# Kernel optimization log

Hardware: AMD Instinct MI355X
Metric: run time of the kernel (lower is better)

The kernel has to match this reference:

```python
import jax, jax.numpy as jnp
import numpy as np

NEG_INF = -9e16
SLOPE = 0.2  # leaky relu slope


def setup_inputs() -> dict:
    key = jax.random.key(0)
    k1, k2, k3, k4 = jax.random.split(key, 4)
    N, F_in, H, D = 3072, 512, 8, 64
    h = jax.random.normal(k1, (N, F_in), dtype=jnp.float32)
    adj = jax.random.randint(k2, (N, N), 0, 2, dtype=jnp.int32)
    W = jax.random.normal(k3, (H, F_in, D), dtype=jnp.float32) * (2.0 / (F_in + D)) ** 0.5
    a = jax.random.normal(k4, (H, 2 * D, 1), dtype=jnp.float32) * (2.0 / (2 * D + 1)) ** 0.5
    return {"h": h, "adj": adj, "W": W, "a": a}


def reference(h, adj, W, a):
    # h: [N, F], W: [H, F, D], a: [H, 2D, 1], adj: [N, N]
    H, _, D = W.shape
    ht = jnp.einsum("nf,hfd->hnd", h, W)            # [H, N, D]
    a_src = a[:, :D, 0]                               # [H, D]
    a_dst = a[:, D:, 0]                               # [H, D]
    src = jnp.einsum("hnd,hd->hn", ht, a_src)        # [H, N]
    dst = jnp.einsum("hnd,hd->hn", ht, a_dst)        # [H, N]
    e = src[:, :, None] + dst[:, None, :]             # [H, N, N]
    e = jnp.where(e > 0, e, SLOPE * e)                # leaky relu
    e = jnp.where(adj[None] > 0, e, NEG_INF)
    att = jax.nn.softmax(e, axis=-1)                  # [H, N, N]
    hp = jnp.einsum("hnm,hmd->hnd", att, ht)         # [H, N, D]
    out = jnp.transpose(hp, (1, 0, 2)).reshape(h.shape[0], H * D)  # concat heads
    return (out, att)
```

## Files before the change

kernel.cpp:

```cpp
#include <hip/hip_runtime.h>

#define NN 3072
#define FF 512
#define HH 8
#define DD 64
#define SLOPEV 0.2f
#define CH2 64
#define NC2 (NN/CH2)

typedef __bf16  bf16x8 __attribute__((ext_vector_type(8)));
typedef __bf16  bf16x4 __attribute__((ext_vector_type(4)));
typedef short   s16x8  __attribute__((ext_vector_type(8)));
typedef float   f32x4  __attribute__((ext_vector_type(4)));
typedef unsigned long long u64;

#define MFMA16(a,b,c) __builtin_amdgcn_mfma_f32_16x16x32_bf16((a),(b),(c),0,0,0)

__device__ __forceinline__ short f2bf(float x){ __bf16 b=(__bf16)x; return __builtin_bit_cast(short,b); }
__device__ __forceinline__ float bf2f(short s){ return (float)__builtin_bit_cast(__bf16,s); }
__device__ __forceinline__ bf16x8 ldbf8(const short* p){ return __builtin_bit_cast(bf16x8, *(const s16x8*)p); }

__device__ __forceinline__ void gload16(const void* g, void* l){
  __builtin_amdgcn_global_load_lds(
      (const __attribute__((address_space(1))) void*)(uintptr_t)g,
      (__attribute__((address_space(3))) void*)(uint32_t)(uintptr_t)l, 16, 0, 0);
}

__global__ __launch_bounds__(64) void k_wt(const float* __restrict__ W, const float* __restrict__ a,
    short* __restrict__ wthi, short* __restrict__ wtlo,
    float* __restrict__ wasrc, float* __restrict__ wadst){
  int h = blockIdx.y, f0 = blockIdx.x*8, d = threadIdx.x;
  float asv = a[h*2*DD + d];
  float adv = a[h*2*DD + DD + d];
  s16x8 vh, vl;
  #pragma unroll
  for (int j=0;j<8;j++){
    float v = W[((size_t)h*FF + f0 + j)*DD + d];
    short s = f2bf(v); vh[j]=s; vl[j]=f2bf(v-bf2f(s));
    float ws_ = v*asv, wd_ = v*adv;
    #pragma unroll
    for (int m=1;m<64;m<<=1){ ws_ += __shfl_xor(ws_,m,64); wd_ += __shfl_xor(wd_,m,64); }
    if (d==0){ wasrc[h*FF+f0+j]=ws_; wadst[h*FF+f0+j]=wd_; }
  }
  size_t o = ((size_t)h*DD + d)*FF + f0;
  *(s16x8*)(wthi+o)=vh; *(s16x8*)(wtlo+o)=vl;
}

__global__ __launch_bounds__(256) void k_pack(const int* __restrict__ adj, u64* __restrict__ padj){
  const int total = NN*NN;
  for (int idx = blockIdx.x*256 + threadIdx.x; idx < total; idx += gridDim.x*256){
    u64 b = __ballot(adj[idx] > 0);
    if ((threadIdx.x & 63) == 0) padj[idx>>6] = b;
  }
}

__global__ __launch_bounds__(256) void k_srcdst(const float* __restrict__ h,
    const float* __restrict__ wasrc, const float* __restrict__ wadst,
    float* __restrict__ src, float* __restrict__ dst){
  int n = blockIdx.x*4 + (threadIdx.x>>6);
  int lane = threadIdx.x & 63;
  const float* hp = h + (size_t)n*FF + lane*8;
  float4 x0 = *(const float4*)hp, x1 = *(const float4*)(hp+4);
  float xs[8] = {x0.x,x0.y,x0.z,x0.w,x1.x,x1.y,x1.z,x1.w};
  float ps[HH], pd[HH];
  #pragma unroll
  for (int hh=0; hh<HH; hh++){
    const float* sp = wasrc + (size_t)hh*FF + lane*8;
    const float* dp = wadst + (size_t)hh*FF + lane*8;
    float4 s0 = *(const float4*)sp, s1 = *(const float4*)(sp+4);
    float4 t0 = *(const float4*)dp, t1 = *(const float4*)(dp+4);
    ps[hh] = xs[0]*s0.x + xs[1]*s0.y + xs[2]*s0.z + xs[3]*s0.w
           + xs[4]*s1.x + xs[5]*s1.y + xs[6]*s1.z + xs[7]*s1.w;
    pd[hh] = xs[0]*t0.x + xs[1]*t0.y + xs[2]*t0.z + xs[3]*t0.w
           + xs[4]*t1.x + xs[5]*t1.y + xs[6]*t1.z + xs[7]*t1.w;
  }
  #pragma unroll
  for (int m=1;m<64;m<<=1){
    #pragma unroll
    for (int hh=0; hh<HH; hh++){ ps[hh] += __shfl_xor(ps[hh],m,64); pd[hh] += __shfl_xor(pd[hh],m,64); }
  }
  if (lane==0){
    #pragma unroll
    for (int hh=0; hh<HH; hh++){ src[hh*NN+n]=ps[hh]; dst[hh*NN+n]=pd[hh]; }
  }
}

__global__ __launch_bounds__(128) void k_ht(const float* __restrict__ h,
    const short* __restrict__ wthi, const short* __restrict__ wtlo,
    short* __restrict__ hthi){
  __shared__ short tH[64][40];
  int hh = blockIdx.y, n0 = blockIdx.x*32;
  int w = threadIdx.x>>6, lane = threadIdx.x&63;
  int r15 = lane&15, g = lane>>4;
  int arow = n0 + w*16 + r15;
  f32x4 acc[4] = {{0.f,0.f,0.f,0.f},{0.f,0.f,0.f,0.f},{0.f,0.f,0.f,0.f},{0.f,0.f,0.f,0.f}};
  const float* ha = h + (size_t)arow*FF + g*8;
  for (int kk=0; kk<FF; kk+=32){
    float4 x0 = *(const float4*)(ha+kk), x1 = *(const float4*)(ha+kk+4);
    float xv[8] = {x0.x,x0.y,x0.z,x0.w,x1.x,x1.y,x1.z,x1.w};
    bf16x8 ahi, alo;
    #pragma unroll
    for (int e=0;e<8;e++){
      short s = f2bf(xv[e]);
      ahi[e] = __builtin_bit_cast(__bf16, s);
      alo[e] = (__bf16)(xv[e] - bf2f(s));
    }
    #pragma unroll
    for (int c=0;c<4;c++){
      size_t bo = ((size_t)hh*DD + c*16 + r15)*FF + g*8 + kk;
      bf16x8 bh = ldbf8(wthi + bo), bl = ldbf8(wtlo + bo);
      acc[c] = MFMA16(ahi,bh,acc[c]);
      acc[c] = MFMA16(ahi,bl,acc[c]);
      acc[c] = MFMA16(alo,bh,acc[c]);
    }
  }
  #pragma unroll
  for (int c=0;c<4;c++){
    #pragma unroll
    for (int r=0;r<4;r++){
      int dloc = c*16 + r15, nloc = w*16 + g*4 + r;
      tH[dloc][nloc] = f2bf(acc[c][r]);
    }
  }
  __syncthreads();
  int row = threadIdx.x>>1, half = threadIdx.x&1;
  size_t o = ((size_t)hh*DD + row)*NN + n0 + half*16;
  *(s16x8*)(hthi + o)     = *(const s16x8*)&tH[row][half*16];
  *(s16x8*)(hthi + o + 8) = *(const s16x8*)&tH[row][half*16+8];
}

__global__ __launch_bounds__(512, 8) void k_att(const u64* __restrict__ padj,
    const float* __restrict__ src, const float* __restrict__ dst,
    const short* __restrict__ hthi, float* __restrict__ dout){
  __shared__ short hA[64][CH2], hB[64][CH2];
  __shared__ short pA[32][CH2], pB[32][CH2];
  const size_t OUTOFF = (size_t)NN*HH*DD;
  int bid = blockIdx.x;
  int h = bid & 7, n0 = (bid >> 3) * 32;
  int t = threadIdx.x;
  int r = t>>4, j = t&15;
  int nrow = n0 + r;
  float srcv = src[h*NN + nrow];
  const float* dsth = dst + h*NN;
  const u64* arow = padj + (size_t)nrow*(NN/64);

  int wv = t>>6, lane = t&63, r15 = lane&15, g = lane>>4;
  int cblk = wv&3, nh = wv>>2;
  int drow = t>>3;
  int sslot = (t&7) ^ (drow&7);
  const short* gh = hthi + ((size_t)(h*DD) + drow)*NN + sslot*8;

  gload16(gh, &hA[wv*8][0]);

  float psum = 0.f;
  for (int c=0;c<24;c++){
    u64 w0 = arow[c*2], w1 = arow[c*2+1];
    const float* dp = dsth + c*128 + j*4;
    float4 d0 = *(const float4*)dp, d1 = *(const float4*)(dp+64);
    float dj[8] = {d0.x,d0.y,d0.z,d0.w,d1.x,d1.y,d1.z,d1.w};
    #pragma unroll
    for (int e=0;e<8;e++){
      float ev = srcv + dj[e];
      ev = fmaxf(ev, SLOPEV*ev);
      u64 bits = (e<4) ? w0 : w1;
      float p = ((bits >> (j*4 + (e&3))) & 1ull) ? __expf(ev) : 0.f;
      psum += p;
    }
  }
  #pragma unroll
  for (int m=1;m<16;m<<=1) psum += __shfl_xor(psum, m, 64);
  float inv = (psum > 0.f) ? 1.f/psum : (1.f/(float)NN);
  bool am = !(psum > 0.f);

  f32x4 acc = {0.f,0.f,0.f,0.f};
  float* attrow = dout + OUTOFF + ((size_t)(h*NN + nrow))*NN;
  int aoff0 = (cblk*16 + r15)*(CH2*2);
  int boff0 = (nh*16 + r15)*(CH2*2);
  int csw   = (r15&7)<<4;
  int pofs  = r*(CH2*2) + ((j*8) ^ ((r&7)<<4));

  const float* dvp = dsth + j*4;
  u64 bits  = arow[0];
  float4 dv  = *(const float4*)dvp;
  u64 bits1 = arow[1];
  float4 dv1 = *(const float4*)(dvp + CH2);

  #pragma unroll 2
  for (int c=0;c<NC2;c++){
    short (*hc)[CH2] = (c&1)?hB:hA;
    short (*hn)[CH2] = (c&1)?hA:hB;
    short (*pc)[CH2] = (c&1)?pB:pA;

    int cs = (c+1 < NC2) ? c+1 : NC2-1;
    gload16(gh + cs*CH2, &hn[wv*8][0]);
    int cp = (c+2 < NC2) ? c+2 : NC2-1;
    u64 bits2 = arow[cp];
    float4 dv2 = *(const float4*)(dvp + cp*CH2);
    float o[4];
    #pragma unroll
    for (int e=0;e<4;e++){
      float ev = srcv + ((const float*)&dv)[e];
      ev = fmaxf(ev, SLOPEV*ev);
      float p = ((bits >> (j*4 + e)) & 1ull) ? __expf(ev) : 0.f;
      if (am) p = 1.f;
      o[e] = p * inv;
    }
    f32x4 s0 = {o[0],o[1],o[2],o[3]};
    __builtin_nontemporal_store(s0, (f32x4*)(attrow + c*CH2 + j*4));
    bf16x4 pb;
    #pragma unroll
    for (int e=0;e<4;e++) pb[e] = (__bf16)o[e];
    *(bf16x4*)((char*)pc + pofs) = pb;

    __builtin_amdgcn_sched_barrier(0);
    asm volatile("s_waitcnt vmcnt(7) lgkmcnt(0)" ::: "memory");
    __builtin_amdgcn_sched_barrier(0);
    __builtin_amdgcn_s_barrier();
    __builtin_amdgcn_sched_barrier(0);

    const char* hcB = (const char*)hc;
    const char* pcB = (const char*)pc;
    #pragma unroll
    for (int ks=0;ks<2;ks++){
      int kb = (g*16 + ks*64) ^ csw;
      bf16x8 bf = *(const bf16x8*)(pcB + boff0 + kb);
      bf16x8 ah = *(const bf16x8*)(hcB + aoff0 + kb);
      acc = MFMA16(ah, bf, acc);
    }
    asm volatile("" ::: "memory");
    __builtin_amdgcn_s_barrier();
    __builtin_amdgcn_sched_barrier(0);

    bits = bits1; bits1 = bits2;
    dv = dv1; dv1 = dv2;
  }

  int n = n0 + nh*16 + r15;
  size_t ob = (size_t)n*(HH*DD) + h*DD + cblk*16 + g*4;
  __builtin_nontemporal_store(acc, (f32x4*)(dout+ob));
}

extern "C" void kernel_launch(void* const* d_in, const int* in_sizes, int n_in,
                              void* d_out, int out_size, void* d_ws, size_t ws_size,
                              hipStream_t stream) {
  const float* h   = (const float*)d_in[0];
  const int*   adj = (const int*)d_in[1];
  const float* W   = (const float*)d_in[2];
  const float* a   = (const float*)d_in[3];
  float* out = (float*)d_out;

  short* wthi = (short*)d_ws;
  short* wtlo = wthi + (size_t)HH*DD*FF;
  short* hthi = wtlo + (size_t)HH*DD*FF;
  float* wasrc= (float*)(hthi + (size_t)HH*DD*NN);
  float* wadst= wasrc + HH*FF;
  float* srcb = wadst + HH*FF;
  float* dstb = srcb + HH*NN;
  u64*   padj = (u64*)(dstb + HH*NN);

  k_wt    <<<dim3(FF/8, HH), 64, 0, stream>>>(W, a, wthi, wtlo, wasrc, wadst);
  k_pack  <<<dim3(2048), 256, 0, stream>>>(adj, padj);
  k_srcdst<<<dim3(NN/4), 256, 0, stream>>>(h, wasrc, wadst, srcb, dstb);
  k_ht    <<<dim3(NN/32, HH), 128, 0, stream>>>(h, wthi, wtlo, hthi);
  k_att   <<<dim3(NN/32*HH), 512, 0, stream>>>(padj, srcb, dstb, hthi, out);
}
```

Baseline: 153.5 us.

## Permute attention-row store order per row to spread write traffic across channels

```diff
diff --git a/kernel.cpp b/kernel.cpp
--- a/kernel.cpp
+++ b/kernel.cpp
@@ -178,12 +178,13 @@
   int boff0 = (nh*16 + r15)*(CH2*2);
   int csw   = (r15&7)<<4;
   int pofs  = r*(CH2*2) + ((j*8) ^ ((r&7)<<4));
-
+  int phi   = r & 15;
   const float* dvp = dsth + j*4;
-  u64 bits  = arow[0];
-  float4 dv  = *(const float4*)dvp;
-  u64 bits1 = arow[1];
-  float4 dv1 = *(const float4*)(dvp + CH2);
+
+  u64 bM0 = arow[0];
+  float4 dM0 = *(const float4*)dvp;
+  u64 bS0 = arow[phi];
+  float4 dS0 = *(const float4*)(dvp + phi*CH2);
 
   #pragma unroll 2
   for (int c=0;c<NC2;c++){
@@ -191,29 +192,44 @@
     short (*hn)[CH2] = (c&1)?hA:hB;
     short (*pc)[CH2] = (c&1)?pB:pA;
 
-    int cs = (c+1 < NC2) ? c+1 : NC2-1;
-    gload16(gh + cs*CH2, &hn[wv*8][0]);
-    int cp = (c+2 < NC2) ? c+2 : NC2-1;
-    u64 bits2 = arow[cp];
-    float4 dv2 = *(const float4*)(dvp + cp*CH2);
+    int cn = (c+1 < NC2) ? c+1 : NC2-1;
+    gload16(gh + cn*CH2, &hn[wv*8][0]);
+    __builtin_amdgcn_sched_barrier(0);
+    u64 bM1 = arow[cn];
+    float4 dM1 = *(const float4*)(dvp + cn*CH2);
+    int sx1 = (cn & 0x30) | ((cn & 15) ^ phi);
+    u64 bS1 = arow[sx1];
+    float4 dS1 = *(const float4*)(dvp + sx1*CH2);
+
     float o[4];
     #pragma unroll
     for (int e=0;e<4;e++){
-      float ev = srcv + ((const float*)&dv)[e];
+      float ev = srcv + ((const float*)&dM0)[e];
       ev = fmaxf(ev, SLOPEV*ev);
-      float p = ((bits >> (j*4 + e)) & 1ull) ? __expf(ev) : 0.f;
+      float p = ((bM0 >> (j*4 + e)) & 1ull) ? __expf(ev) : 0.f;
       if (am) p = 1.f;
       o[e] = p * inv;
     }
-    f32x4 s0 = {o[0],o[1],o[2],o[3]};
-    __builtin_nontemporal_store(s0, (f32x4*)(attrow + c*CH2 + j*4));
     bf16x4 pb;
     #pragma unroll
     for (int e=0;e<4;e++) pb[e] = (__bf16)o[e];
     *(bf16x4*)((char*)pc + pofs) = pb;
 
-    __builtin_amdgcn_sched_barrier(0);
-    asm volatile("s_waitcnt vmcnt(7) lgkmcnt(0)" ::: "memory");
+    int sxc = (c & 0x30) | ((c & 15) ^ phi);
+    float os[4];
+    #pragma unroll
+    for (int e=0;e<4;e++){
+      float ev = srcv + ((const float*)&dS0)[e];
+      ev = fmaxf(ev, SLOPEV*ev);
+      float p = ((bS0 >> (j*4 + e)) & 1ull) ? __expf(ev) : 0.f;
+      if (am) p = 1.f;
+      os[e] = p * inv;
+    }
+    f32x4 s0 = {os[0],os[1],os[2],os[3]};
+    __builtin_nontemporal_store(s0, (f32x4*)(attrow + sxc*CH2 + j*4));
+
+    __builtin_amdgcn_sched_barrier(0);
+    asm volatile("s_waitcnt vmcnt(11) lgkmcnt(0)" ::: "memory");
     __builtin_amdgcn_sched_barrier(0);
     __builtin_amdgcn_s_barrier();
     __builtin_amdgcn_sched_barrier(0);
@@ -231,8 +247,7 @@
     __builtin_amdgcn_s_barrier();
     __builtin_amdgcn_sched_barrier(0);
 
-    bits = bits1; bits1 = bits2;
-    dv = dv1; dv1 = dv2;
+    bM0 = bM1; dM0 = dM1; bS0 = bS1; dS0 = dS1;
   }
 
   int n = n0 + nh*16 + r15;
```

Result: slower. 164.0 us (+6.8%).

## Split key dimension across waves and compute attention operand directly in registers

Applied to the files above, without the earlier changes.

```diff
diff --git a/kernel.cpp b/kernel.cpp
--- a/kernel.cpp
+++ b/kernel.cpp
@@ -5,26 +5,18 @@
 #define HH 8
 #define DD 64
 #define SLOPEV 0.2f
-#define CH2 64
-#define NC2 (NN/CH2)
 
 typedef __bf16  bf16x8 __attribute__((ext_vector_type(8)));
-typedef __bf16  bf16x4 __attribute__((ext_vector_type(4)));
 typedef short   s16x8  __attribute__((ext_vector_type(8)));
 typedef float   f32x4  __attribute__((ext_vector_type(4)));
 typedef unsigned long long u64;
+typedef unsigned int u32;
 
 #define MFMA16(a,b,c) __builtin_amdgcn_mfma_f32_16x16x32_bf16((a),(b),(c),0,0,0)
 
 __device__ __forceinline__ short f2bf(float x){ __bf16 b=(__bf16)x; return __builtin_bit_cast(short,b); }
 __device__ __forceinline__ float bf2f(short s){ return (float)__builtin_bit_cast(__bf16,s); }
 __device__ __forceinline__ bf16x8 ldbf8(const short* p){ return __builtin_bit_cast(bf16x8, *(const s16x8*)p); }
-
-__device__ __forceinline__ void gload16(const void* g, void* l){
-  __builtin_amdgcn_global_load_lds(
-      (const __attribute__((address_space(1))) void*)(uintptr_t)g,
-      (__attribute__((address_space(3))) void*)(uint32_t)(uintptr_t)l, 16, 0, 0);
-}
 
 __global__ __launch_bounds__(64) void k_wt(const float* __restrict__ W, const float* __restrict__ a,
     short* __restrict__ wthi, short* __restrict__ wtlo,
@@ -132,112 +124,109 @@
 __global__ __launch_bounds__(512, 8) void k_att(const u64* __restrict__ padj,
     const float* __restrict__ src, const float* __restrict__ dst,
     const short* __restrict__ hthi, float* __restrict__ dout){
-  __shared__ short hA[64][CH2], hB[64][CH2];
-  __shared__ short pA[32][CH2], pB[32][CH2];
+  __shared__ float rs[8][16];
+  __shared__ float hpbuf[4][2][16][68];
   const size_t OUTOFF = (size_t)NN*HH*DD;
   int bid = blockIdx.x;
   int h = bid & 7, n0 = (bid >> 3) * 32;
-  int t = threadIdx.x;
-  int r = t>>4, j = t&15;
-  int nrow = n0 + r;
-  float srcv = src[h*NN + nrow];
+  int t = threadIdx.x, wv = t>>6, lane = t&63;
+  int r15 = lane&15, g = lane>>4;
+  int rg = wv&1, mq = wv>>1;
+  int prow = n0 + rg*16 + r15;
+  float srcv = src[h*NN + prow];
   const float* dsth = dst + h*NN;
-  const u64* arow = padj + (size_t)nrow*(NN/64);
-
-  int wv = t>>6, lane = t&63, r15 = lane&15, g = lane>>4;
-  int cblk = wv&3, nh = wv>>2;
-  int drow = t>>3;
-  int sslot = (t&7) ^ (drow&7);
-  const short* gh = hthi + ((size_t)(h*DD) + drow)*NN + sslot*8;
-
-  gload16(gh, &hA[wv*8][0]);
+  const u32* abits = (const u32*)(padj + (size_t)prow*(NN/64));
+  const int mq24 = mq*24, mq768 = mq*768;
 
   float psum = 0.f;
-  for (int c=0;c<24;c++){
-    u64 w0 = arow[c*2], w1 = arow[c*2+1];
-    const float* dp = dsth + c*128 + j*4;
-    float4 d0 = *(const float4*)dp, d1 = *(const float4*)(dp+64);
+  #pragma unroll 2
+  for (int s=0;s<24;s++){
+    u32 bits = abits[mq24+s];
+    const float* dp = dsth + mq768 + s*32 + g*8;
+    float4 d0 = *(const float4*)dp, d1 = *(const float4*)(dp+4);
     float dj[8] = {d0.x,d0.y,d0.z,d0.w,d1.x,d1.y,d1.z,d1.w};
     #pragma unroll
     for (int e=0;e<8;e++){
       float ev = srcv + dj[e];
       ev = fmaxf(ev, SLOPEV*ev);
-      u64 bits = (e<4) ? w0 : w1;
-      float p = ((bits >> (j*4 + (e&3))) & 1ull) ? __expf(ev) : 0.f;
-      psum += p;
-    }
-  }
-  #pragma unroll
-  for (int m=1;m<16;m<<=1) psum += __shfl_xor(psum, m, 64);
-  float inv = (psum > 0.f) ? 1.f/psum : (1.f/(float)NN);
-  bool am = !(psum > 0.f);
-
-  f32x4 acc = {0.f,0.f,0.f,0.f};
-  float* attrow = dout + OUTOFF + ((size_t)(h*NN + nrow))*NN;
-  int aoff0 = (cblk*16 + r15)*(CH2*2);
-  int boff0 = (nh*16 + r15)*(CH2*2);
-  int csw   = (r15&7)<<4;
-  int pofs  = r*(CH2*2) + ((j*8) ^ ((r&7)<<4));
-
-  const float* dvp = dsth + j*4;
-  u64 bits  = arow[0];
-  float4 dv  = *(const float4*)dvp;
-  u64 bits1 = arow[1];
-  float4 dv1 = *(const float4*)(dvp + CH2);
+      psum += ((bits >> (g*8+e)) & 1u) ? __expf(ev) : 0.f;
+    }
+  }
+  psum += __shfl_xor(psum,16,64); psum += __shfl_xor(psum,32,64);
+  if (lane < 16) rs[wv][lane] = psum;
+  __syncthreads();
+  float tot = rs[rg][r15] + rs[2+rg][r15] + rs[4+rg][r15] + rs[6+rg][r15];
+  float inv = (tot > 0.f) ? 1.f/tot : (1.f/(float)NN);
+  bool am = !(tot > 0.f);
+
+  f32x4 acc[4] = {{0.f,0.f,0.f,0.f},{0.f,0.f,0.f,0.f},{0.f,0.f,0.f,0.f},{0.f,0.f,0.f,0.f}};
+  float* attrow = dout + OUTOFF + ((size_t)(h*NN + prow))*NN + mq768;
+  const short* gb = hthi + ((size_t)(h*DD) + r15)*NN + mq768 + g*8;
 
   #pragma unroll 2
-  for (int c=0;c<NC2;c++){
-    short (*hc)[CH2] = (c&1)?hB:hA;
-    short (*hn)[CH2] = (c&1)?hA:hB;
-    short (*pc)[CH2] = (c&1)?pB:pA;
-
-    int cs = (c+1 < NC2) ? c+1 : NC2-1;
-    gload16(gh + cs*CH2, &hn[wv*8][0]);
-    int cp = (c+2 < NC2) ? c+2 : NC2-1;
-    u64 bits2 = arow[cp];
-    float4 dv2 = *(const float4*)(dvp + cp*CH2);
-    float o[4];
+  for (int s=0;s<24;s++){
+    int mb = s*32;
+    u32 bits = abits[mq24+s];
+    const float* dpa = dsth + mq768 + mb;
+    float4 dsa = *(const float4*)(dpa + g*4);
+    float4 dsb = *(const float4*)(dpa + 16 + g*4);
+    float4 dma = *(const float4*)(dpa + g*8);
+    float4 dmb = *(const float4*)(dpa + g*8 + 4);
+
+    f32x4 o0, o1;
     #pragma unroll
     for (int e=0;e<4;e++){
-      float ev = srcv + ((const float*)&dv)[e];
+      float ev = srcv + ((const float*)&dsa)[e];
       ev = fmaxf(ev, SLOPEV*ev);
-      float p = ((bits >> (j*4 + e)) & 1ull) ? __expf(ev) : 0.f;
+      float p = ((bits >> (g*4+e)) & 1u) ? __expf(ev) : 0.f;
       if (am) p = 1.f;
-      o[e] = p * inv;
-    }
-    f32x4 s0 = {o[0],o[1],o[2],o[3]};
-    __builtin_nontemporal_store(s0, (f32x4*)(attrow + c*CH2 + j*4));
-    bf16x4 pb;
-    #pragma unroll
-    for (int e=0;e<4;e++) pb[e] = (__bf16)o[e];
-    *(bf16x4*)((char*)pc + pofs) = pb;
-
-    __builtin_amdgcn_sched_barrier(0);
-    asm volatile("s_waitcnt vmcnt(7) lgkmcnt(0)" ::: "memory");
-    __builtin_amdgcn_sched_barrier(0);
-    __builtin_amdgcn_s_barrier();
-    __builtin_amdgcn_sched_barrier(0);
-
-    const char* hcB = (const char*)hc;
-    const char* pcB = (const char*)pc;
-    #pragma unroll
-    for (int ks=0;ks<2;ks++){
-      int kb = (g*16 + ks*64) ^ csw;
-      bf16x8 bf = *(const bf16x8*)(pcB + boff0 + kb);
-      bf16x8 ah = *(const bf16x8*)(hcB + aoff0 + kb);
-      acc = MFMA16(ah, bf, acc);
-    }
-    asm volatile("" ::: "memory");
-    __builtin_amdgcn_s_barrier();
-    __builtin_amdgcn_sched_barrier(0);
-
-    bits = bits1; bits1 = bits2;
-    dv = dv1; dv1 = dv2;
-  }
-
-  int n = n0 + nh*16 + r15;
-  size_t ob = (size_t)n*(HH*DD) + h*DD + cblk*16 + g*4;
-  __builtin_nontemporal_store(acc, (f32x4*)(dout+ob));
+      o0[e] = p * inv;
+      float ev2 = srcv + ((const float*)&dsb)[e];
+      ev2 = fmaxf(ev2, SLOPEV*ev2);
+      float p2 = ((bits >> (16+g*4+e)) & 1u) ? __expf(ev2) : 0.f;
+      if (am) p2 = 1.f;
+      o1[e] = p2 * inv;
+    }
+    __builtin_nontemporal_store(o0, (f32x4*)(attrow + mb + g*4));
+    __builtin_nontemporal_store(o1, (f32x4*)(attrow + mb + 16 + g*4));
+
+    bf16x8 af;
+    #pragma unroll
+    for (int e=0;e<4;e++){
+      float ev = srcv + ((const float*)&dma)[e];
+      ev = fmaxf(ev, SLOPEV*ev);
+      float p = ((bits >> (g*8+e)) & 1u) ? __expf(ev) : 0.f;
+      if (am) p = 1.f;
+      af[e] = (__bf16)(p * inv);
+      float ev2 = srcv + ((const float*)&dmb)[e];
+      ev2 = fmaxf(ev2, SLOPEV*ev2);
+      float p2 = ((bits >> (g*8+4+e)) & 1u) ? __expf(ev2) : 0.f;
+      if (am) p2 = 1.f;
+      af[4+e] = (__bf16)(p2 * inv);
+    }
+    #pragma unroll
+    for (int cb=0;cb<4;cb++){
+      bf16x8 bh = ldbf8(gb + (size_t)cb*16*NN + mb);
+      acc[cb] = MFMA16(af, bh, acc[cb]);
+    }
+  }
+
+  #pragma unroll
+  for (int cb=0;cb<4;cb++){
+    #pragma unroll
+    for (int reg=0;reg<4;reg++)
+      hpbuf[mq][rg][g*4+reg][cb*16+r15] = acc[cb][reg];
+  }
+  __syncthreads();
+  int orow = t>>4, dc = (t&15)*4;
+  int org = orow>>4, orr = orow&15;
+  f32x4 osum;
+  #pragma unroll
+  for (int k=0;k<4;k++)
+    osum[k] = hpbuf[0][org][orr][dc+k] + hpbuf[1][org][orr][dc+k]
+            + hpbuf[2][org][orr][dc+k] + hpbuf[3][org][orr][dc+k];
+  size_t ob = (size_t)(n0+orow)*(HH*DD) + h*DD + dc;
+  __builtin_nontemporal_store(osum, (f32x4*)(dout+ob));
 }
 
 extern "C" void kernel_launch(void* const* d_in, const int* in_sizes, int n_in,
```

Result: slower. 203.9 us (+32.8%).

## Merge prep kernels into two launches and double attention chunk size

Applied to the files above, without the earlier changes.

```diff
diff --git a/kernel.cpp b/kernel.cpp
--- a/kernel.cpp
+++ b/kernel.cpp
@@ -5,8 +5,8 @@
 #define HH 8
 #define DD 64
 #define SLOPEV 0.2f
-#define CH2 64
-#define NC2 (NN/CH2)
+#define CH 128
+#define NC (NN/CH)
 
 typedef __bf16  bf16x8 __attribute__((ext_vector_type(8)));
 typedef __bf16  bf16x4 __attribute__((ext_vector_type(4)));
@@ -26,114 +26,119 @@
       (__attribute__((address_space(3))) void*)(uint32_t)(uintptr_t)l, 16, 0, 0);
 }
 
-__global__ __launch_bounds__(64) void k_wt(const float* __restrict__ W, const float* __restrict__ a,
+__global__ __launch_bounds__(256) void k_prep1(const float* __restrict__ W, const float* __restrict__ a,
+    const int* __restrict__ adj,
     short* __restrict__ wthi, short* __restrict__ wtlo,
-    float* __restrict__ wasrc, float* __restrict__ wadst){
-  int h = blockIdx.y, f0 = blockIdx.x*8, d = threadIdx.x;
-  float asv = a[h*2*DD + d];
-  float adv = a[h*2*DD + DD + d];
-  s16x8 vh, vl;
-  #pragma unroll
-  for (int j=0;j<8;j++){
-    float v = W[((size_t)h*FF + f0 + j)*DD + d];
-    short s = f2bf(v); vh[j]=s; vl[j]=f2bf(v-bf2f(s));
-    float ws_ = v*asv, wd_ = v*adv;
-    #pragma unroll
-    for (int m=1;m<64;m<<=1){ ws_ += __shfl_xor(ws_,m,64); wd_ += __shfl_xor(wd_,m,64); }
-    if (d==0){ wasrc[h*FF+f0+j]=ws_; wadst[h*FF+f0+j]=wd_; }
-  }
-  size_t o = ((size_t)h*DD + d)*FF + f0;
-  *(s16x8*)(wthi+o)=vh; *(s16x8*)(wtlo+o)=vl;
-}
-
-__global__ __launch_bounds__(256) void k_pack(const int* __restrict__ adj, u64* __restrict__ padj){
-  const int total = NN*NN;
-  for (int idx = blockIdx.x*256 + threadIdx.x; idx < total; idx += gridDim.x*256){
-    u64 b = __ballot(adj[idx] > 0);
-    if ((threadIdx.x & 63) == 0) padj[idx>>6] = b;
-  }
-}
-
-__global__ __launch_bounds__(256) void k_srcdst(const float* __restrict__ h,
+    float* __restrict__ wasrc, float* __restrict__ wadst, u64* __restrict__ padj){
+  int bid = blockIdx.x, t = threadIdx.x;
+  if (bid < 128){
+    int uid = bid*4 + (t>>6);
+    int h = uid>>6, f0 = (uid&63)*8, d = t&63;
+    float asv = a[h*2*DD + d];
+    float adv = a[h*2*DD + DD + d];
+    s16x8 vh, vl;
+    #pragma unroll
+    for (int j=0;j<8;j++){
+      float v = W[((size_t)h*FF + f0 + j)*DD + d];
+      short s = f2bf(v); vh[j]=s; vl[j]=f2bf(v-bf2f(s));
+      float ws_ = v*asv, wd_ = v*adv;
+      #pragma unroll
+      for (int m=1;m<64;m<<=1){ ws_ += __shfl_xor(ws_,m,64); wd_ += __shfl_xor(wd_,m,64); }
+      if (d==0){ wasrc[h*FF+f0+j]=ws_; wadst[h*FF+f0+j]=wd_; }
+    }
+    size_t o = ((size_t)h*DD + d)*FF + f0;
+    *(s16x8*)(wthi+o)=vh; *(s16x8*)(wtlo+o)=vl;
+  } else {
+    const int total = NN*NN;
+    for (int idx = (bid-128)*256 + t; idx < total; idx += 1024*256){
+      u64 b = __ballot(adj[idx] > 0);
+      if ((t & 63) == 0) padj[idx>>6] = b;
+    }
+  }
+}
+
+__global__ __launch_bounds__(256) void k_prep2(const float* __restrict__ h,
+    const short* __restrict__ wthi, const short* __restrict__ wtlo,
     const float* __restrict__ wasrc, const float* __restrict__ wadst,
-    float* __restrict__ src, float* __restrict__ dst){
-  int n = blockIdx.x*4 + (threadIdx.x>>6);
-  int lane = threadIdx.x & 63;
-  const float* hp = h + (size_t)n*FF + lane*8;
-  float4 x0 = *(const float4*)hp, x1 = *(const float4*)(hp+4);
-  float xs[8] = {x0.x,x0.y,x0.z,x0.w,x1.x,x1.y,x1.z,x1.w};
-  float ps[HH], pd[HH];
-  #pragma unroll
-  for (int hh=0; hh<HH; hh++){
-    const float* sp = wasrc + (size_t)hh*FF + lane*8;
-    const float* dp = wadst + (size_t)hh*FF + lane*8;
-    float4 s0 = *(const float4*)sp, s1 = *(const float4*)(sp+4);
-    float4 t0 = *(const float4*)dp, t1 = *(const float4*)(dp+4);
-    ps[hh] = xs[0]*s0.x + xs[1]*s0.y + xs[2]*s0.z + xs[3]*s0.w
-           + xs[4]*s1.x + xs[5]*s1.y + xs[6]*s1.z + xs[7]*s1.w;
-    pd[hh] = xs[0]*t0.x + xs[1]*t0.y + xs[2]*t0.z + xs[3]*t0.w
-           + xs[4]*t1.x + xs[5]*t1.y + xs[6]*t1.z + xs[7]*t1.w;
-  }
-  #pragma unroll
-  for (int m=1;m<64;m<<=1){
-    #pragma unroll
-    for (int hh=0; hh<HH; hh++){ ps[hh] += __shfl_xor(ps[hh],m,64); pd[hh] += __shfl_xor(pd[hh],m,64); }
-  }
-  if (lane==0){
-    #pragma unroll
-    for (int hh=0; hh<HH; hh++){ src[hh*NN+n]=ps[hh]; dst[hh*NN+n]=pd[hh]; }
-  }
-}
-
-__global__ __launch_bounds__(128) void k_ht(const float* __restrict__ h,
-    const short* __restrict__ wthi, const short* __restrict__ wtlo,
-    short* __restrict__ hthi){
-  __shared__ short tH[64][40];
-  int hh = blockIdx.y, n0 = blockIdx.x*32;
-  int w = threadIdx.x>>6, lane = threadIdx.x&63;
-  int r15 = lane&15, g = lane>>4;
-  int arow = n0 + w*16 + r15;
-  f32x4 acc[4] = {{0.f,0.f,0.f,0.f},{0.f,0.f,0.f,0.f},{0.f,0.f,0.f,0.f},{0.f,0.f,0.f,0.f}};
-  const float* ha = h + (size_t)arow*FF + g*8;
-  for (int kk=0; kk<FF; kk+=32){
-    float4 x0 = *(const float4*)(ha+kk), x1 = *(const float4*)(ha+kk+4);
-    float xv[8] = {x0.x,x0.y,x0.z,x0.w,x1.x,x1.y,x1.z,x1.w};
-    bf16x8 ahi, alo;
-    #pragma unroll
-    for (int e=0;e<8;e++){
-      short s = f2bf(xv[e]);
-      ahi[e] = __builtin_bit_cast(__bf16, s);
-      alo[e] = (__bf16)(xv[e] - bf2f(s));
+    float* __restrict__ src, float* __restrict__ dst, short* __restrict__ hthi){
+  __shared__ short tH[2][64][40];
+  int bid = blockIdx.x, t = threadIdx.x;
+  if (bid < 768){
+    int n = bid*4 + (t>>6);
+    int lane = t & 63;
+    const float* hp = h + (size_t)n*FF + lane*8;
+    float4 x0 = *(const float4*)hp, x1 = *(const float4*)(hp+4);
+    float xs[8] = {x0.x,x0.y,x0.z,x0.w,x1.x,x1.y,x1.z,x1.w};
+    float ps[HH], pd[HH];
+    #pragma unroll
+    for (int hh=0; hh<HH; hh++){
+      const float* sp = wasrc + (size_t)hh*FF + lane*8;
+      const float* dp = wadst + (size_t)hh*FF + lane*8;
+      float4 s0 = *(const float4*)sp, s1 = *(const float4*)(sp+4);
+      float4 t0 = *(const float4*)dp, t1 = *(const float4*)(dp+4);
+      ps[hh] = xs[0]*s0.x + xs[1]*s0.y + xs[2]*s0.z + xs[3]*s0.w
+             + xs[4]*s1.x + xs[5]*s1.y + xs[6]*s1.z + xs[7]*s1.w;
+      pd[hh] = xs[0]*t0.x + xs[1]*t0.y + xs[2]*t0.z + xs[3]*t0.w
+             + xs[4]*t1.x + xs[5]*t1.y + xs[6]*t1.z + xs[7]*t1.w;
+    }
+    #pragma unroll
+    for (int m=1;m<64;m<<=1){
+      #pragma unroll
+      for (int hh=0; hh<HH; hh++){ ps[hh] += __shfl_xor(ps[hh],m,64); pd[hh] += __shfl_xor(pd[hh],m,64); }
+    }
+    if (lane==0){
+      #pragma unroll
+      for (int hh=0; hh<HH; hh++){ src[hh*NN+n]=ps[hh]; dst[hh*NN+n]=pd[hh]; }
+    }
+  } else {
+    int uu = t>>7, tid = t&127;
+    int unit = (bid-768)*2 + uu;
+    int hh = unit/96, n0 = (unit%96)*32;
+    int w = tid>>6, lane = tid&63;
+    int r15 = lane&15, g = lane>>4;
+    int arow = n0 + w*16 + r15;
+    f32x4 acc[4] = {{0.f,0.f,0.f,0.f},{0.f,0.f,0.f,0.f},{0.f,0.f,0.f,0.f},{0.f,0.f,0.f,0.f}};
+    const float* ha = h + (size_t)arow*FF + g*8;
+    for (int kk=0; kk<FF; kk+=32){
+      float4 x0 = *(const float4*)(ha+kk), x1 = *(const float4*)(ha+kk+4);
+      float xv[8] = {x0.x,x0.y,x0.z,x0.w,x1.x,x1.y,x1.z,x1.w};
+      bf16x8 ahi, alo;
+      #pragma unroll
+      for (int e=0;e<8;e++){
+        short s = f2bf(xv[e]);
+        ahi[e] = __builtin_bit_cast(__bf16, s);
+        alo[e] = (__bf16)(xv[e] - bf2f(s));
+      }
+      #pragma unroll
+      for (int c=0;c<4;c++){
+        size_t bo = ((size_t)hh*DD + c*16 + r15)*FF + g*8 + kk;
+        bf16x8 bh = ldbf8(wthi + bo), bl = ldbf8(wtlo + bo);
+        acc[c] = MFMA16(ahi,bh,acc[c]);
+        acc[c] = MFMA16(ahi,bl,acc[c]);
+        acc[c] = MFMA16(alo,bh,acc[c]);
+      }
     }
     #pragma unroll
     for (int c=0;c<4;c++){
-      size_t bo = ((size_t)hh*DD + c*16 + r15)*FF + g*8 + kk;
-      bf16x8 bh = ldbf8(wthi + bo), bl = ldbf8(wtlo + bo);
-      acc[c] = MFMA16(ahi,bh,acc[c]);
-      acc[c] = MFMA16(ahi,bl,acc[c]);
-      acc[c] = MFMA16(alo,bh,acc[c]);
-    }
-  }
-  #pragma unroll
-  for (int c=0;c<4;c++){
-    #pragma unroll
-    for (int r=0;r<4;r++){
-      int dloc = c*16 + r15, nloc = w*16 + g*4 + r;
-      tH[dloc][nloc] = f2bf(acc[c][r]);
-    }
-  }
-  __syncthreads();
-  int row = threadIdx.x>>1, half = threadIdx.x&1;
-  size_t o = ((size_t)hh*DD + row)*NN + n0 + half*16;
-  *(s16x8*)(hthi + o)     = *(const s16x8*)&tH[row][half*16];
-  *(s16x8*)(hthi + o + 8) = *(const s16x8*)&tH[row][half*16+8];
-}
-
-__global__ __launch_bounds__(512, 8) void k_att(const u64* __restrict__ padj,
+      #pragma unroll
+      for (int r=0;r<4;r++){
+        int dloc = c*16 + r15, nloc = w*16 + g*4 + r;
+        tH[uu][dloc][nloc] = f2bf(acc[c][r]);
+      }
+    }
+    __syncthreads();
+    int row = tid>>1, half = tid&1;
+    size_t o = ((size_t)hh*DD + row)*NN + n0 + half*16;
+    *(s16x8*)(hthi + o)     = *(const s16x8*)&tH[uu][row][half*16];
+    *(s16x8*)(hthi + o + 8) = *(const s16x8*)&tH[uu][row][half*16+8];
+  }
+}
+
+__global__ __launch_bounds__(512, 6) void k_att(const u64* __restrict__ padj,
     const float* __restrict__ src, const float* __restrict__ dst,
     const short* __restrict__ hthi, float* __restrict__ dout){
-  __shared__ short hA[64][CH2], hB[64][CH2];
-  __shared__ short pA[32][CH2], pB[32][CH2];
+  __shared__ short hA[64][CH], hB[64][CH];
+  __shared__ short pA[32][CH], pB[32][CH];
   const size_t OUTOFF = (size_t)NN*HH*DD;
   int bid = blockIdx.x;
   int h = bid & 7, n0 = (bid >> 3) * 32;
@@ -146,16 +151,18 @@
 
   int wv = t>>6, lane = t&63, r15 = lane&15, g = lane>>4;
   int cblk = wv&3, nh = wv>>2;
-  int drow = t>>3;
-  int sslot = (t&7) ^ (drow&7);
-  const short* gh = hthi + ((size_t)(h*DD) + drow)*NN + sslot*8;
-
-  gload16(gh, &hA[wv*8][0]);
+  int drow = t>>4;
+  int sslot = (t&15) ^ (drow&7);
+  const short* ghA = hthi + ((size_t)(h*DD) + drow)*NN + sslot*8;
+  const short* ghB = hthi + ((size_t)(h*DD) + drow + 32)*NN + sslot*8;
+
+  gload16(ghA, &hA[wv*4][0]);
+  gload16(ghB, &hA[32 + wv*4][0]);
 
   float psum = 0.f;
-  for (int c=0;c<24;c++){
+  for (int c=0;c<NC;c++){
     u64 w0 = arow[c*2], w1 = arow[c*2+1];
-    const float* dp = dsth + c*128 + j*4;
+    const float* dp = dsth + c*CH + j*4;
     float4 d0 = *(const float4*)dp, d1 = *(const float4*)(dp+64);
     float dj[8] = {d0.x,d0.y,d0.z,d0.w,d1.x,d1.y,d1.z,d1.w};
     #pragma unroll
@@ -174,46 +181,56 @@
 
   f32x4 acc = {0.f,0.f,0.f,0.f};
   float* attrow = dout + OUTOFF + ((size_t)(h*NN + nrow))*NN;
-  int aoff0 = (cblk*16 + r15)*(CH2*2);
-  int boff0 = (nh*16 + r15)*(CH2*2);
+  int aoff0 = (cblk*16 + r15)*(CH*2);
+  int boff0 = (nh*16 + r15)*(CH*2);
   int csw   = (r15&7)<<4;
-  int pofs  = r*(CH2*2) + ((j*8) ^ ((r&7)<<4));
-
+  int xw    = (r&7)<<4;
+  int pof0  = r*(CH*2) + ((j*8) ^ xw);
+  int pof1  = r*(CH*2) + ((128 + j*8) ^ xw);
   const float* dvp = dsth + j*4;
-  u64 bits  = arow[0];
-  float4 dv  = *(const float4*)dvp;
-  u64 bits1 = arow[1];
-  float4 dv1 = *(const float4*)(dvp + CH2);
-
-  #pragma unroll 2
-  for (int c=0;c<NC2;c++){
-    short (*hc)[CH2] = (c&1)?hB:hA;
-    short (*hn)[CH2] = (c&1)?hA:hB;
-    short (*pc)[CH2] = (c&1)?pB:pA;
-
-    int cs = (c+1 < NC2) ? c+1 : NC2-1;
-    gload16(gh + cs*CH2, &hn[wv*8][0]);
-    int cp = (c+2 < NC2) ? c+2 : NC2-1;
-    u64 bits2 = arow[cp];
-    float4 dv2 = *(const float4*)(dvp + cp*CH2);
-    float o[4];
+
+  u64 w0 = arow[0], w1 = arow[1];
+  float4 dva = *(const float4*)dvp;
+  float4 dvb = *(const float4*)(dvp + 64);
+
+  for (int c=0;c<NC;c++){
+    short (*hc)[CH] = (c&1)?hB:hA;
+    short (*hn)[CH] = (c&1)?hA:hB;
+    short (*pc)[CH] = (c&1)?pB:pA;
+
+    int cn = (c+1 < NC) ? c+1 : NC-1;
+    gload16(ghA + cn*CH, &hn[wv*4][0]);
+    gload16(ghB + cn*CH, &hn[32 + wv*4][0]);
+    u64 w0n = arow[cn*2], w1n = arow[cn*2+1];
+    float4 dva_n = *(const float4*)(dvp + cn*CH);
+    float4 dvb_n = *(const float4*)(dvp + cn*CH + 64);
+
+    float o[8];
     #pragma unroll
     for (int e=0;e<4;e++){
-      float ev = srcv + ((const float*)&dv)[e];
+      float ev = srcv + ((const float*)&dva)[e];
       ev = fmaxf(ev, SLOPEV*ev);
-      float p = ((bits >> (j*4 + e)) & 1ull) ? __expf(ev) : 0.f;
+      float p = ((w0 >> (j*4 + e)) & 1ull) ? __expf(ev) : 0.f;
       if (am) p = 1.f;
       o[e] = p * inv;
+      float ev2 = srcv + ((const float*)&dvb)[e];
+      ev2 = fmaxf(ev2, SLOPEV*ev2);
+      float p2 = ((w1 >> (j*4 + e)) & 1ull) ? __expf(ev2) : 0.f;
+      if (am) p2 = 1.f;
+      o[4+e] = p2 * inv;
     }
     f32x4 s0 = {o[0],o[1],o[2],o[3]};
-    __builtin_nontemporal_store(s0, (f32x4*)(attrow + c*CH2 + j*4));
-    bf16x4 pb;
-    #pragma unroll
-    for (int e=0;e<4;e++) pb[e] = (__bf16)o[e];
-    *(bf16x4*)((char*)pc + pofs) = pb;
-
-    __builtin_amdgcn_sched_barrier(0);
-    asm volatile("s_waitcnt vmcnt(7) lgkmcnt(0)" ::: "memory");
+    f32x4 s1 = {o[4],o[5],o[6],o[7]};
+    __builtin_nontemporal_store(s0, (f32x4*)(attrow + c*CH + j*4));
+    __builtin_nontemporal_store(s1, (f32x4*)(attrow + c*CH + 64 + j*4));
+    bf16x4 p0, p1;
+    #pragma unroll
+    for (int e=0;e<4;e++){ p0[e] = (__bf16)o[e]; p1[e] = (__bf16)o[4+e]; }
+    *(bf16x4*)((char*)pc + pof0) = p0;
+    *(bf16x4*)((char*)pc + pof1) = p1;
+
+    __builtin_amdgcn_sched_barrier(0);
+    asm volatile("s_waitcnt vmcnt(12) lgkmcnt(0)" ::: "memory");
     __builtin_amdgcn_sched_barrier(0);
     __builtin_amdgcn_s_barrier();
     __builtin_amdgcn_sched_barrier(0);
@@ -221,8 +238,8 @@
     const char* hcB = (const char*)hc;
     const char* pcB = (const char*)pc;
     #pragma unroll
-    for (int ks=0;ks<2;ks++){
-      int kb = (g*16 + ks*64) ^ csw;
+    for (int ks=0;ks<4;ks++){
+      int kb = (ks*64 + g*16) ^ csw;
       bf16x8 bf = *(const bf16x8*)(pcB + boff0 + kb);
       bf16x8 ah = *(const bf16x8*)(hcB + aoff0 + kb);
       acc = MFMA16(ah, bf, acc);
@@ -231,8 +248,7 @@
     __builtin_amdgcn_s_barrier();
     __builtin_amdgcn_sched_barrier(0);
 
-    bits = bits1; bits1 = bits2;
-    dv = dv1; dv1 = dv2;
+    w0 = w0n; w1 = w1n; dva = dva_n; dvb = dvb_n;
   }
 
   int n = n0 + nh*16 + r15;
@@ -258,9 +274,7 @@
   float* dstb = srcb + HH*NN;
   u64*   padj = (u64*)(dstb + HH*NN);
 
-  k_wt    <<<dim3(FF/8, HH), 64, 0, stream>>>(W, a, wthi, wtlo, wasrc, wadst);
-  k_pack  <<<dim3(2048), 256, 0, stream>>>(adj, padj);
-  k_srcdst<<<dim3(NN/4), 256, 0, stream>>>(h, wasrc, wadst, srcb, dstb);
-  k_ht    <<<dim3(NN/32, HH), 128, 0, stream>>>(h, wthi, wtlo, hthi);
-  k_att   <<<dim3(NN/32*HH), 512, 0, stream>>>(padj, srcb, dstb, hthi, out);
-}
+  k_prep1<<<dim3(1152), 256, 0, stream>>>(W, a, adj, wthi, wtlo, wasrc, wadst, padj);
+  k_prep2<<<dim3(1152), 256, 0, stream>>>(h, wthi, wtlo, wasrc, wadst, srcb, dstb, hthi);
+  k_att  <<<dim3(NN/32*HH), 512, 0, stream>>>(padj, srcb, dstb, hthi, out);
+}
```

Measured after the change: 139.9 us. -8.9%, faster.
